# Kernel optimization log

Hardware: AMD Instinct MI355X
Metric: run time of the kernel (lower is better)

The kernel has to match this reference:

```python
import jax, jax.numpy as jnp
import numpy as np

N, E = 20000, 200000
HID, NH, L = 128, 8, 7
DH = HID // NH
SCALE = float(np.sqrt(DH))
NNUM = 5
MLP_IN = HID + HID + 8 + 8 + 8 + NNUM  # 285
EPS = 1e-5


def _ln(x, g, b):
    mu = jnp.mean(x, -1, keepdims=True)
    var = jnp.mean((x - mu) ** 2, -1, keepdims=True)
    return (x - mu) * jax.lax.rsqrt(var + EPS) * g + b


def setup_inputs() -> dict:
    key = jax.random.key(0)
    ks = jax.random.split(key, 24)
    f = lambda k, s: (0.05 * jax.random.normal(k, s)).astype(jnp.float32)
    z = lambda s: jnp.zeros(s, jnp.float32)
    o = lambda s: jnp.ones(s, jnp.float32)
    inp = {
        'node_feats': f(ks[0], (N, 2)),
        'numericals': f(ks[1], (E, NNUM)),
        'W_emb': f(ks[2], (2, HID)), 'b_emb': z((HID,)),
        'WQ': f(ks[3], (L, HID, HID)), 'bQ': z((L, HID)),
        'WK': f(ks[4], (L, HID, HID)), 'bK': z((L, HID)),
        'WV': f(ks[5], (L, HID, HID)), 'bV': z((L, HID)),
        'WO': f(ks[6], (L, HID, HID)), 'bO': z((L, HID)),
        'ln1_g': o((L, HID)), 'ln1_b': z((L, HID)),
        'ln2_g': o((L, HID)), 'ln2_b': z((L, HID)),
        'W1': f(ks[7], (L, HID, HID)), 'b1': z((L, HID)),
        'W2': f(ks[8], (L, HID, HID)), 'b2': z((L, HID)),
        'curr_emb': f(ks[9], (15, 8)), 'pay_emb': f(ks[10], (7, 8)),
        'mlp_Wh': f(ks[11], (3, MLP_IN, MLP_IN)), 'mlp_bh': z((3, MLP_IN)),
        'mlp_Wo': f(ks[12], (MLP_IN, 2)), 'mlp_bo': z((2,)),
        'src': jax.random.randint(ks[13], (E,), 0, N, dtype=jnp.int32),
        'dst': jax.random.randint(ks[14], (E,), 0, N, dtype=jnp.int32),
        'payment_currency': jax.random.randint(ks[15], (E,), 0, 15, dtype=jnp.int32),
        'receiving_currency': jax.random.randint(ks[16], (E,), 0, 15, dtype=jnp.int32),
        'payment_format': jax.random.randint(ks[17], (E,), 0, 7, dtype=jnp.int32),
    }
    return inp


def reference(node_feats, numericals, W_emb, b_emb, WQ, bQ, WK, bK, WV, bV, WO, bO,
              ln1_g, ln1_b, ln2_g, ln2_b, W1, b1, W2, b2, curr_emb, pay_emb,
              mlp_Wh, mlp_bh, mlp_Wo, mlp_bo, src, dst,
              payment_currency, receiving_currency, payment_format):
    h = node_feats @ W_emb + b_emb  # [N, HID]
    for l in range(L):
        # --- graph multi-head attention (segment softmax over in-edges of dst) ---
        x = _ln(h, ln1_g[l], ln1_b[l])
        Q = (x @ WQ[l] + bQ[l]).reshape(N, NH, DH)
        K = (x @ WK[l] + bK[l]).reshape(N, NH, DH)
        V = (x @ WV[l] + bV[l]).reshape(N, NH, DH)
        scores = jnp.einsum('ehd,ehd->eh', Q[dst], K[src]) / SCALE  # [E, NH]
        m = jax.ops.segment_max(scores, dst, num_segments=N)        # [N, NH]
        ex = jnp.exp(scores - m[dst])
        den = jax.ops.segment_sum(ex, dst, num_segments=N)
        w = ex / den[dst]                                           # attn weights per edge
        attn = jax.ops.segment_sum(w[:, :, None] * V[src], dst, num_segments=N)
        h = h + attn.reshape(N, HID) @ WO[l] + bO[l]
        # --- FFN ---
        x = _ln(h, ln2_g[l], ln2_b[l])
        h = h + jax.nn.relu(x @ W1[l] + b1[l]) @ W2[l] + b2[l]
    # --- edge classifier ---
    ef = jnp.concatenate([curr_emb[payment_currency], curr_emb[receiving_currency],
                          pay_emb[payment_format], numericals], axis=1)  # [E, 29]
    y = jnp.concatenate([h[src], h[dst], ef], axis=1)  # [E, 285]
    for i in range(3):
        y = jax.nn.relu(y @ mlp_Wh[i] + mlp_bh[i])
    return y @ mlp_Wo + mlp_bo  # [E, 2]
```

## Files before the change

### kernel.cpp

```cpp
#include <hip/hip_runtime.h>

#define HID 128
#define NH 8
#define DH 16
#define NLAYERS 7
#define MLP_IN 285
#define MP 288
#define LDW 296
#define XS 136

typedef short short8 __attribute__((ext_vector_type(8)));
typedef float f32x4 __attribute__((ext_vector_type(4)));
typedef float f32x16 __attribute__((ext_vector_type(16)));
typedef unsigned short ushort8 __attribute__((ext_vector_type(8)));

__device__ inline unsigned short f2bf(float f) {
    union { float f; unsigned int u; } v; v.f = f;
    unsigned int r = v.u + 0x7FFF + ((v.u >> 16) & 1);
    return (unsigned short)(r >> 16);
}
__device__ inline float bf2f(unsigned short u) {
    union { unsigned int u; float f; } v; v.u = ((unsigned int)u) << 16;
    return v.f;
}

__global__ __launch_bounds__(256) void embed_kernel(
    const float* __restrict__ nf, const float* __restrict__ We,
    const float* __restrict__ be, float* __restrict__ h, int N)
{
    int idx = blockIdx.x * 256 + threadIdx.x;
    if (idx >= N * HID) return;
    int n = idx >> 7, j = idx & 127;
    h[idx] = fmaf(nf[n * 2], We[j], fmaf(nf[n * 2 + 1], We[HID + j], be[j]));
}

__global__ __launch_bounds__(256) void prep_nodew_kernel(
    const float* __restrict__ WQ, const float* __restrict__ WK,
    const float* __restrict__ WV, const float* __restrict__ WO,
    const float* __restrict__ W1, const float* __restrict__ W2,
    unsigned short* __restrict__ wnh, unsigned short* __restrict__ wnl)
{
    int idx = blockIdx.x * 256 + threadIdx.x;
    if (idx >= 42 * 32 * 64) return;
    int lane = idx & 63;
    int r = idx >> 6;
    int kt = r & 7; r >>= 3;
    int ct = r & 3; r >>= 2;
    int m = r;
    int l = m / 6, wi = m - l * 6;
    const float* Wb;
    switch (wi) {
        case 0: Wb = WQ; break; case 1: Wb = WK; break; case 2: Wb = WV; break;
        case 3: Wb = WO; break; case 4: Wb = W1; break; default: Wb = W2; break;
    }
    Wb += (size_t)l * HID * HID;
    int n = ct * 32 + (lane & 31);
    int kb = kt * 16 + (lane >> 5) * 8;
    ushort8 vh, vl;
#pragma unroll
    for (int j = 0; j < 8; ++j) {
        float w = Wb[(size_t)(kb + j) * HID + n];
        unsigned short hi = f2bf(w);
        vh[j] = hi;
        vl[j] = f2bf(w - bf2f(hi));
    }
    *(ushort8*)&wnh[(size_t)idx * 8] = vh;
    *(ushort8*)&wnl[(size_t)idx * 8] = vl;
}

#define LOADB(m, BH, BL) do { \
    size_t fb_ = (((size_t)(matbase + (m)) * 32 + (size_t)wave * 8) * 64 + lane) * 8; \
    const unsigned short* Bh_ = wnh + fb_; \
    const unsigned short* Bl_ = wnl + fb_; \
    _Pragma("unroll") \
    for (int kt = 0; kt < 8; ++kt) { \
        BH[kt] = *(const short8*)&Bh_[kt * 512]; \
        BL[kt] = *(const short8*)&Bl_[kt * 512]; \
    } \
} while (0)

#define COMPACC(BH, BL) \
    f32x16 acc = {}; \
    _Pragma("unroll") \
    for (int kt = 0; kt < 8; ++kt) \
        acc = __builtin_amdgcn_mfma_f32_32x32x16_bf16(ah[kt], BH[kt], acc, 0, 0, 0); \
    _Pragma("unroll") \
    for (int kt = 0; kt < 8; ++kt) \
        acc = __builtin_amdgcn_mfma_f32_32x32x16_bf16(al[kt], BH[kt], acc, 0, 0, 0); \
    _Pragma("unroll") \
    for (int kt = 0; kt < 8; ++kt) \
        acc = __builtin_amdgcn_mfma_f32_32x32x16_bf16(ah[kt], BL[kt], acc, 0, 0, 0);

__global__ __launch_bounds__(256, 2) void ln_qkv_mfma(
    const float* __restrict__ h,
    const float* __restrict__ g, const float* __restrict__ bb,
    const unsigned short* __restrict__ wnh, const unsigned short* __restrict__ wnl,
    int matbase,
    const float* __restrict__ bQ, const float* __restrict__ bK, const float* __restrict__ bV,
    float* __restrict__ qo, float* __restrict__ kvo, int M)
{
    __shared__ unsigned short Xh[32][XS];
    __shared__ unsigned short Xl[32][XS];
    int tid = threadIdx.x;
    int lane = tid & 63, wave = tid >> 6;
    int rowBase = blockIdx.x * 32;

    for (int i = 0; i < 8; ++i) {
        int r = wave * 8 + i;
        int row = rowBase + r;
        float a0 = 0.f, a1 = 0.f;
        if (row < M) {
            a0 = h[(size_t)row * HID + lane];
            a1 = h[(size_t)row * HID + 64 + lane];
        }
        float s = a0 + a1;
#pragma unroll
        for (int off = 32; off > 0; off >>= 1) s += __shfl_down(s, off, 64);
        s = __shfl(s, 0, 64);
        float mu = s * (1.0f / 128.0f);
        float d0 = a0 - mu, d1 = a1 - mu;
        float v = d0 * d0 + d1 * d1;
#pragma unroll
        for (int off = 32; off > 0; off >>= 1) v += __shfl_down(v, off, 64);
        v = __shfl(v, 0, 64);
        float rr = rsqrtf(v * (1.0f / 128.0f) + 1e-5f);
        float x0 = d0 * rr * g[lane] + bb[lane];
        float x1 = d1 * rr * g[64 + lane] + bb[64 + lane];
        unsigned short h0 = f2bf(x0), h1 = f2bf(x1);
        Xh[r][lane] = h0;           Xh[r][64 + lane] = h1;
        Xl[r][lane] = f2bf(x0 - bf2f(h0));
        Xl[r][64 + lane] = f2bf(x1 - bf2f(h1));
    }
    __syncthreads();

    int l31 = lane & 31;
    int half = lane >> 5;

    short8 ah[8], al[8];
#pragma unroll
    for (int kt = 0; kt < 8; ++kt) {
        ah[kt] = *(const short8*)&Xh[l31][kt * 16 + half * 8];
        al[kt] = *(const short8*)&Xl[l31][kt * 16 + half * 8];
    }

    int col = wave * 32 + l31;
    int kvpos = (col >> 1) * 4 + (col & 1);

    short8 bh0[8], bl0[8], bh1[8], bl1[8];
    LOADB(0, bh0, bl0);
    LOADB(1, bh1, bl1);
    {
        COMPACC(bh0, bl0);
        float bv = bQ[col];
#pragma unroll
        for (int r = 0; r < 16; ++r) {
            int rowm = (r & 3) + 8 * (r >> 2) + 4 * half;
            int row = rowBase + rowm;
            if (row < M) qo[(size_t)row * HID + col] = acc[r] + bv;
        }
    }
    LOADB(2, bh0, bl0);
    {
        COMPACC(bh1, bl1);
        float bv = bK[col];
#pragma unroll
        for (int r = 0; r < 16; ++r) {
            int rowm = (r & 3) + 8 * (r >> 2) + 4 * half;
            int row = rowBase + rowm;
            if (row < M) kvo[(size_t)row * 256 + kvpos] = acc[r] + bv;
        }
    }
    {
        COMPACC(bh0, bl0);
        float bv = bV[col];
#pragma unroll
        for (int r = 0; r < 16; ++r) {
            int rowm = (r & 3) + 8 * (r >> 2) + 4 * half;
            int row = rowBase + rowm;
            if (row < M) kvo[(size_t)row * 256 + kvpos + 2] = acc[r] + bv;
        }
    }
}

__global__ __launch_bounds__(256, 2) void post_mfma(
    const float* __restrict__ at, const float* __restrict__ hin,
    const unsigned short* __restrict__ wnh, const unsigned short* __restrict__ wnl,
    int matbase,
    const float* __restrict__ bO,
    const float* __restrict__ g2, const float* __restrict__ b2g,
    const float* __restrict__ b1, const float* __restrict__ b2,
    float* __restrict__ hout, int M)
{
    __shared__ unsigned short Ah[32][XS];
    __shared__ unsigned short Al[32][XS];
    __shared__ unsigned short Th[32][XS];
    __shared__ unsigned short Tl[32][XS];
    __shared__ float Hs[32][132];
    int tid = threadIdx.x;
    int lane = tid & 63, wave = tid >> 6;
    int rowBase = blockIdx.x * 32;
    int l31 = lane & 31;
    int half = lane >> 5;

    for (int i = tid; i < 32 * 32; i += 256) {
        int r = i >> 5, c4 = i & 31;
        int row = rowBase + r;
        float4 va = make_float4(0.f, 0.f, 0.f, 0.f), vh = va;
        if (row < M) {
            va = *(const float4*)&at[(size_t)row * HID + c4 * 4];
            vh = *(const float4*)&hin[(size_t)row * HID + c4 * 4];
        }
        const float* vp = (const float*)&va;
#pragma unroll
        for (int q = 0; q < 4; ++q) {
            unsigned short hi = f2bf(vp[q]);
            Ah[r][c4 * 4 + q] = hi;
            Al[r][c4 * 4 + q] = f2bf(vp[q] - bf2f(hi));
        }
        *(float4*)&Hs[r][c4 * 4] = vh;
    }
    __syncthreads();

    int colW = wave * 32 + l31;

    {
        short8 ah[8], al[8];
#pragma unroll
        for (int kt = 0; kt < 8; ++kt) {
            ah[kt] = *(const short8*)&Ah[l31][kt * 16 + half * 8];
            al[kt] = *(const short8*)&Al[l31][kt * 16 + half * 8];
        }
        short8 bh[8], bl[8];
        LOADB(3, bh, bl);
        COMPACC(bh, bl);
        float bv = bO[colW];
#pragma unroll
        for (int r = 0; r < 16; ++r) {
            int rowm = (r & 3) + 8 * (r >> 2) + 4 * half;
            Hs[rowm][colW] += acc[r] + bv;
        }
    }
    __syncthreads();

    for (int i = 0; i < 8; ++i) {
        int r = wave * 8 + i;
        float a0 = Hs[r][lane];
        float a1 = Hs[r][64 + lane];
        float s = a0 + a1;
#pragma unroll
        for (int off = 32; off > 0; off >>= 1) s += __shfl_down(s, off, 64);
        s = __shfl(s, 0, 64);
        float mu = s * (1.0f / 128.0f);
        float d0 = a0 - mu, d1 = a1 - mu;
        float v = d0 * d0 + d1 * d1;
#pragma unroll
        for (int off = 32; off > 0; off >>= 1) v += __shfl_down(v, off, 64);
        v = __shfl(v, 0, 64);
        float rr = rsqrtf(v * (1.0f / 128.0f) + 1e-5f);
        float x0 = d0 * rr * g2[lane] + b2g[lane];
        float x1 = d1 * rr * g2[64 + lane] + b2g[64 + lane];
        unsigned short h0 = f2bf(x0), h1 = f2bf(x1);
        Ah[r][lane] = h0;           Ah[r][64 + lane] = h1;
        Al[r][lane] = f2bf(x0 - bf2f(h0));
        Al[r][64 + lane] = f2bf(x1 - bf2f(h1));
    }
    __syncthreads();

    {
        short8 ah[8], al[8];
#pragma unroll
        for (int kt = 0; kt < 8; ++kt) {
            ah[kt] = *(const short8*)&Ah[l31][kt * 16 + half * 8];
            al[kt] = *(const short8*)&Al[l31][kt * 16 + half * 8];
        }
        short8 bh[8], bl[8];
        LOADB(4, bh, bl);
        COMPACC(bh, bl);
        float bv = b1[colW];
#pragma unroll
        for (int r = 0; r < 16; ++r) {
            int rowm = (r & 3) + 8 * (r >> 2) + 4 * half;
            float t = fmaxf(acc[r] + bv, 0.f);
            unsigned short hi = f2bf(t);
            Th[rowm][colW] = hi;
            Tl[rowm][colW] = f2bf(t - bf2f(hi));
        }
    }
    __syncthreads();

    {
        short8 ah[8], al[8];
#pragma unroll
        for (int kt = 0; kt < 8; ++kt) {
            ah[kt] = *(const short8*)&Th[l31][kt * 16 + half * 8];
            al[kt] = *(const short8*)&Tl[l31][kt * 16 + half * 8];
        }
        short8 bh[8], bl[8];
        LOADB(5, bh, bl);
        COMPACC(bh, bl);
        float bv = b2[colW];
#pragma unroll
        for (int r = 0; r < 16; ++r) {
            int rowm = (r & 3) + 8 * (r >> 2) + 4 * half;
            int row = rowBase + rowm;
            if (row < M)
                hout[(size_t)row * HID + colW] = Hs[rowm][colW] + acc[r] + bv;
        }
    }
}

__global__ __launch_bounds__(256) void deg_kernel(
    const int* __restrict__ dst, int* __restrict__ deg, int E)
{
    int e = blockIdx.x * 256 + threadIdx.x;
    if (e < E) atomicAdd(&deg[dst[e]], 1);
}

__global__ __launch_bounds__(256) void scan_kernel(
    const int* __restrict__ deg, int* __restrict__ rowptr,
    int* __restrict__ cursor, int N)
{
    __shared__ int sums[256];
    int tid = threadIdx.x;
    int chunk = (N + 255) / 256;
    int lo = tid * chunk;
    int hi = lo + chunk; if (hi > N) hi = N;
    int s = 0;
    for (int i = lo; i < hi && i >= 0; ++i) s += deg[i];
    sums[tid] = s;
    __syncthreads();
    for (int off = 1; off < 256; off <<= 1) {
        int v = (tid >= off) ? sums[tid - off] : 0;
        __syncthreads();
        sums[tid] += v;
        __syncthreads();
    }
    int base = (tid == 0) ? 0 : sums[tid - 1];
    for (int i = lo; i < hi; ++i) {
        rowptr[i] = base; cursor[i] = base; base += deg[i];
    }
    if (tid == 255) rowptr[N] = sums[255];
}

__global__ __launch_bounds__(256) void scatter_kernel(
    const int* __restrict__ src, const int* __restrict__ dst,
    int* __restrict__ cursor, int* __restrict__ ssrc, int E)
{
    int e = blockIdx.x * 256 + threadIdx.x;
    if (e < E) {
        int p = atomicAdd(&cursor[dst[e]], 1);
        ssrc[p] = src[e];
    }
}

__global__ __launch_bounds__(256) void attn_fused_kernel(
    const float* __restrict__ q, const float* __restrict__ kv,
    const int* __restrict__ rowptr, const int* __restrict__ ssrc,
    float* __restrict__ at, int N)
{
    int node = blockIdx.x * 4 + (threadIdx.x >> 6);
    int lane = threadIdx.x & 63;
    if (node >= N) return;
    int beg = rowptr[node], end = rowptr[node + 1];
    float2 q2 = *(const float2*)&q[(size_t)node * HID + lane * 2];
    float ax = 0.f, ay = 0.f, den = 0.f;
    int i = beg;
    for (; i + 2 <= end; i += 2) {
        int s0 = ssrc[i], s1 = ssrc[i + 1];
        float4 kv0 = *(const float4*)&kv[(size_t)s0 * 256 + lane * 4];
        float4 kv1 = *(const float4*)&kv[(size_t)s1 * 256 + lane * 4];
        float p0 = fmaf(q2.x, kv0.x, q2.y * kv0.y);
        float p1 = fmaf(q2.x, kv1.x, q2.y * kv1.y);
        p0 += __shfl_xor(p0, 1, 64); p1 += __shfl_xor(p1, 1, 64);
        p0 += __shfl_xor(p0, 2, 64); p1 += __shfl_xor(p1, 2, 64);
        p0 += __shfl_xor(p0, 4, 64); p1 += __shfl_xor(p1, 4, 64);
        float w0 = __expf(p0 * 0.25f);
        float w1 = __expf(p1 * 0.25f);
        den += w0 + w1;
        ax = fmaf(w1, kv1.z, fmaf(w0, kv0.z, ax));
        ay = fmaf(w1, kv1.w, fmaf(w0, kv0.w, ay));
    }
    if (i < end) {
        int s = ssrc[i];
        float4 kv0 = *(const float4*)&kv[(size_t)s * 256 + lane * 4];
        float p0 = fmaf(q2.x, kv0.x, q2.y * kv0.y);
        p0 += __shfl_xor(p0, 1, 64);
        p0 += __shfl_xor(p0, 2, 64);
        p0 += __shfl_xor(p0, 4, 64);
        float w0 = __expf(p0 * 0.25f);
        den += w0;
        ax = fmaf(w0, kv0.z, ax);
        ay = fmaf(w0, kv0.w, ay);
    }
    float inv = (den > 0.f) ? 1.f / den : 0.f;
    float2 o; o.x = ax * inv; o.y = ay * inv;
    *(float2*)&at[(size_t)node * HID + lane * 2] = o;
}

__global__ __launch_bounds__(256) void prep_wp_kernel(
    const float* __restrict__ Wh, unsigned short* __restrict__ wp)
{
    int idx = blockIdx.x * 256 + threadIdx.x;
    if (idx >= 3 * 9 * 18 * 64) return;
    int lane = idx & 63;
    int r = idx >> 6;
    int kt = r % 18; r /= 18;
    int ct = r % 9;
    int layer = r / 9;
    int n = ct * 32 + (lane & 31);
    int kbase = kt * 16 + (lane >> 5) * 8;
    ushort8 val;
#pragma unroll
    for (int j = 0; j < 8; ++j) {
        int k = kbase + j;
        float v = (n < MLP_IN && k < MLP_IN)
            ? Wh[(size_t)layer * MLP_IN * MLP_IN + (size_t)k * MLP_IN + n] : 0.f;
        val[j] = f2bf(v);
    }
    *(ushort8*)&wp[(size_t)idx * 8] = val;
}

__global__ __launch_bounds__(256) void prep_hb_kernel(
    const float* __restrict__ h, unsigned short* __restrict__ hb, int n)
{
    int idx = blockIdx.x * 256 + threadIdx.x;
    if (idx >= n) return;
    hb[idx] = f2bf(h[idx]);
}

#define ELOADH(h, BUF) do { \
    const unsigned short* Wp_ = Wb + (size_t)((h) >> 1) * 9216 + (size_t)((h) & 1) * 9 * 512; \
    _Pragma("unroll") \
    for (int j = 0; j < 9; ++j) BUF[j] = *(const short8*)&Wp_[j * 512]; \
    __builtin_amdgcn_sched_barrier(0); \
} while (0)

__global__ __launch_bounds__(256, 2) void edge_mlp_mfma(
    const unsigned short* __restrict__ hb, const float* __restrict__ ce,
    const float* __restrict__ pe, const float* __restrict__ num,
    const int* __restrict__ src, const int* __restrict__ dst,
    const int* __restrict__ pc, const int* __restrict__ rc,
    const int* __restrict__ pf,
    const unsigned short* __restrict__ wp, const float* __restrict__ bh,
    const float* __restrict__ Wo, const float* __restrict__ bo,
    float* __restrict__ out, int E)
{
    __shared__ unsigned short y[128 * LDW];
    int tid = threadIdx.x;
    int e0 = blockIdx.x * 128;

    for (int i = tid; i < 128 * 36; i += 256) {
        int t = i / 36;
        int c = i - t * 36;
        int e = e0 + t;
        if (e >= E) e = E - 1;
        ushort8 val;
        if (c < 16) {
            val = *(const ushort8*)&hb[(size_t)src[e] * HID + c * 8];
        } else if (c < 32) {
            val = *(const ushort8*)&hb[(size_t)dst[e] * HID + (c - 16) * 8];
        } else if (c == 32) {
            const float* p = &ce[pc[e] * 8];
#pragma unroll
            for (int j = 0; j < 8; ++j) val[j] = f2bf(p[j]);
        } else if (c == 33) {
            const float* p = &ce[rc[e] * 8];
#pragma unroll
            for (int j = 0; j < 8; ++j) val[j] = f2bf(p[j]);
        } else if (c == 34) {
            const float* p = &pe[pf[e] * 8];
#pragma unroll
            for (int j = 0; j < 8; ++j) val[j] = f2bf(p[j]);
        } else {
            const float* p = &num[(size_t)e * 5];
#pragma unroll
            for (int j = 0; j < 5; ++j) val[j] = f2bf(p[j]);
            val[5] = 0; val[6] = 0; val[7] = 0;
        }
        *(ushort8*)&y[t * LDW + c * 8] = val;
    }
    __syncthreads();

    int wave = tid >> 6;
    int lane = tid & 63;
    int l31 = lane & 31;
    int half = lane >> 5;
    int rowA = wave * 32 + l31;

    for (int layer = 0; layer < 3; ++layer) {
        const unsigned short* __restrict__ Wl = wp + (size_t)layer * 9 * 18 * 64 * 8;
        const float* __restrict__ bias = bh + layer * MLP_IN;
        const unsigned short* Wb = Wl + (size_t)lane * 8;

        short8 afr[18];
#pragma unroll
        for (int kt = 0; kt < 18; ++kt)
            afr[kt] = *(const short8*)&y[rowA * LDW + kt * 16 + half * 8];
        __syncthreads();

        short8 bA[9], bB[9];
        ELOADH(0, bA);
#pragma unroll
        for (int ct = 0; ct < 9; ++ct) {
            f32x16 acc = {};
            ELOADH(2 * ct + 1, bB);
#pragma unroll
            for (int j = 0; j < 9; ++j)
                acc = __builtin_amdgcn_mfma_f32_32x32x16_bf16(afr[j], bA[j], acc, 0, 0, 0);
            if (ct < 8) ELOADH(2 * ct + 2, bA);
#pragma unroll
            for (int j = 0; j < 9; ++j)
                acc = __builtin_amdgcn_mfma_f32_32x32x16_bf16(afr[9 + j], bB[j], acc, 0, 0, 0);
            int col = ct * 32 + l31;
            if (col < MLP_IN) {
                float bv = bias[col];
#pragma unroll
                for (int r = 0; r < 16; ++r) {
                    int rowm = (r & 3) + 8 * (r >> 2) + 4 * half;
                    y[(wave * 32 + rowm) * LDW + col] = f2bf(fmaxf(acc[r] + bv, 0.f));
                }
            }
        }
        __syncthreads();
    }

    {
        int t = tid >> 1, oc = tid & 1;
        int e = e0 + t;
        if (e < E) {
            const unsigned short* yr = &y[t * LDW];
            float p0 = 0.f, p1 = 0.f, p2 = 0.f, p3 = 0.f;
            for (int kc = 0; kc < 35; ++kc) {
                ushort8 yv = *(const ushort8*)&yr[kc * 8];
                int kb = kc * 8;
                p0 = fmaf(bf2f(yv[0]), Wo[(kb + 0) * 2 + oc], p0);
                p1 = fmaf(bf2f(yv[1]), Wo[(kb + 1) * 2 + oc], p1);
                p2 = fmaf(bf2f(yv[2]), Wo[(kb + 2) * 2 + oc], p2);
                p3 = fmaf(bf2f(yv[3]), Wo[(kb + 3) * 2 + oc], p3);
                p0 = fmaf(bf2f(yv[4]), Wo[(kb + 4) * 2 + oc], p0);
                p1 = fmaf(bf2f(yv[5]), Wo[(kb + 5) * 2 + oc], p1);
                p2 = fmaf(bf2f(yv[6]), Wo[(kb + 6) * 2 + oc], p2);
                p3 = fmaf(bf2f(yv[7]), Wo[(kb + 7) * 2 + oc], p3);
            }
            float acc = bo[oc] + (p0 + p1) + (p2 + p3);
            for (int k = 280; k < MLP_IN; ++k)
                acc = fmaf(bf2f(yr[k]), Wo[k * 2 + oc], acc);
            out[(size_t)e * 2 + oc] = acc;
        }
    }
}

extern "C" void kernel_launch(void* const* d_in, const int* in_sizes, int n_in,
                              void* d_out, int out_size, void* d_ws, size_t ws_size,
                              hipStream_t stream)
{
    const float* node_feats = (const float*)d_in[0];
    const float* numericals = (const float*)d_in[1];
    const float* W_emb = (const float*)d_in[2];
    const float* b_emb = (const float*)d_in[3];
    const float* WQ = (const float*)d_in[4];
    const float* bQ = (const float*)d_in[5];
    const float* WK = (const float*)d_in[6];
    const float* bK = (const float*)d_in[7];
    const float* WV = (const float*)d_in[8];
    const float* bV = (const float*)d_in[9];
    const float* WO = (const float*)d_in[10];
    const float* bO = (const float*)d_in[11];
    const float* ln1_g = (const float*)d_in[12];
    const float* ln1_b = (const float*)d_in[13];
    const float* ln2_g = (const float*)d_in[14];
    const float* ln2_b = (const float*)d_in[15];
    const float* W1 = (const float*)d_in[16];
    const float* b1 = (const float*)d_in[17];
    const float* W2 = (const float*)d_in[18];
    const float* b2 = (const float*)d_in[19];
    const float* curr_emb = (const float*)d_in[20];
    const float* pay_emb = (const float*)d_in[21];
    const float* mlp_Wh = (const float*)d_in[22];
    const float* mlp_bh = (const float*)d_in[23];
    const float* mlp_Wo = (const float*)d_in[24];
    const float* mlp_bo = (const float*)d_in[25];
    const int* src = (const int*)d_in[26];
    const int* dst = (const int*)d_in[27];
    const int* pc = (const int*)d_in[28];
    const int* rc = (const int*)d_in[29];
    const int* pf = (const int*)d_in[30];

    const int N = in_sizes[0] / 2;
    const int E = in_sizes[26];

    float* ws = (float*)d_ws;
    float* h   = ws;
    float* qb  = h   + (size_t)N * HID;
    float* kvb = qb  + (size_t)N * HID;
    float* at  = kvb + (size_t)N * HID * 2;
    unsigned short* hb = (unsigned short*)(at + (size_t)N * HID);
    unsigned short* wpk = hb + (size_t)N * HID;
    unsigned short* wnh = wpk + (size_t)3 * 9 * 18 * 64 * 8;
    unsigned short* wnl = wnh + (size_t)42 * 32 * 64 * 8;
    int* rowptr = (int*)(wnl + (size_t)42 * 32 * 64 * 8);
    int* deg    = rowptr + (N + 1);
    int* cursor = deg + N;
    int* ssrc   = cursor + N;

    prep_wp_kernel<<<(3 * 9 * 18 * 64 + 255) / 256, 256, 0, stream>>>(mlp_Wh, wpk);
    prep_nodew_kernel<<<(42 * 32 * 64 + 255) / 256, 256, 0, stream>>>(
        WQ, WK, WV, WO, W1, W2, wnh, wnl);

    embed_kernel<<<(N * HID + 255) / 256, 256, 0, stream>>>(node_feats, W_emb, b_emb, h, N);

    hipMemsetAsync(deg, 0, (size_t)N * sizeof(int), stream);
    deg_kernel<<<(E + 255) / 256, 256, 0, stream>>>(dst, deg, E);
    scan_kernel<<<1, 256, 0, stream>>>(deg, rowptr, cursor, N);
    scatter_kernel<<<(E + 255) / 256, 256, 0, stream>>>(src, dst, cursor, ssrc, E);

    int nodeBlocks = (N + 31) / 32;

    for (int l = 0; l < NLAYERS; ++l) {
        ln_qkv_mfma<<<nodeBlocks, 256, 0, stream>>>(
            h, ln1_g + l * HID, ln1_b + l * HID,
            wnh, wnl, l * 6,
            bQ + l * HID, bK + l * HID, bV + l * HID,
            qb, kvb, N);

        attn_fused_kernel<<<(N + 3) / 4, 256, 0, stream>>>(qb, kvb, rowptr, ssrc, at, N);

        post_mfma<<<nodeBlocks, 256, 0, stream>>>(
            at, h, wnh, wnl, l * 6,
            bO + l * HID,
            ln2_g + l * HID, ln2_b + l * HID,
            b1 + l * HID, b2 + l * HID,
            h, N);
    }

    prep_hb_kernel<<<(N * HID + 255) / 256, 256, 0, stream>>>(h, hb, N * HID);

    edge_mlp_mfma<<<(E + 127) / 128, 256, 0, stream>>>(
        hb, curr_emb, pay_emb, numericals, src, dst, pc, rc, pf,
        wpk, mlp_bh, mlp_Wo, mlp_bo, (float*)d_out, E);
}
```

Baseline: 1.063 ms.

## Fuse attention, output/FFN and next-layer LN+QKV into one per-layer kernel

```diff
diff --git a/kernel.cpp b/kernel.cpp
--- a/kernel.cpp
+++ b/kernel.cpp
@@ -182,14 +182,19 @@
     }
 }
 
-__global__ __launch_bounds__(256, 2) void post_mfma(
-    const float* __restrict__ at, const float* __restrict__ hin,
+__global__ __launch_bounds__(256, 2) void attn_post_qkv(
+    const float* __restrict__ qin, const float* __restrict__ kvin,
+    const int* __restrict__ rowptr, const int* __restrict__ ssrc,
+    float* __restrict__ h,
     const unsigned short* __restrict__ wnh, const unsigned short* __restrict__ wnl,
     int matbase,
     const float* __restrict__ bO,
     const float* __restrict__ g2, const float* __restrict__ b2g,
     const float* __restrict__ b1, const float* __restrict__ b2,
-    float* __restrict__ hout, int M)
+    int doQKV,
+    const float* __restrict__ g1n, const float* __restrict__ b1n,
+    const float* __restrict__ bQn, const float* __restrict__ bKn, const float* __restrict__ bVn,
+    float* __restrict__ qo, float* __restrict__ kvo, int M)
 {
     __shared__ unsigned short Ah[32][XS];
     __shared__ unsigned short Al[32][XS];
@@ -205,19 +210,54 @@
     for (int i = tid; i < 32 * 32; i += 256) {
         int r = i >> 5, c4 = i & 31;
         int row = rowBase + r;
-        float4 va = make_float4(0.f, 0.f, 0.f, 0.f), vh = va;
-        if (row < M) {
-            va = *(const float4*)&at[(size_t)row * HID + c4 * 4];
-            vh = *(const float4*)&hin[(size_t)row * HID + c4 * 4];
-        }
-        const float* vp = (const float*)&va;
-#pragma unroll
-        for (int q = 0; q < 4; ++q) {
-            unsigned short hi = f2bf(vp[q]);
-            Ah[r][c4 * 4 + q] = hi;
-            Al[r][c4 * 4 + q] = f2bf(vp[q] - bf2f(hi));
-        }
+        float4 vh = (row < M) ? *(const float4*)&h[(size_t)row * HID + c4 * 4]
+                              : make_float4(0.f, 0.f, 0.f, 0.f);
         *(float4*)&Hs[r][c4 * 4] = vh;
+    }
+
+    for (int nn = 0; nn < 8; ++nn) {
+        int r = nn * 4 + wave;
+        int node = rowBase + r;
+        float ax = 0.f, ay = 0.f, den = 0.f;
+        if (node < M) {
+            float2 q2 = *(const float2*)&qin[(size_t)node * HID + lane * 2];
+            int beg = rowptr[node], end = rowptr[node + 1];
+            int i = beg;
+            for (; i + 2 <= end; i += 2) {
+                int s0 = ssrc[i], s1 = ssrc[i + 1];
+                float4 kv0 = *(const float4*)&kvin[(size_t)s0 * 256 + lane * 4];
+                float4 kv1 = *(const float4*)&kvin[(size_t)s1 * 256 + lane * 4];
+                float p0 = fmaf(q2.x, kv0.x, q2.y * kv0.y);
+                float p1 = fmaf(q2.x, kv1.x, q2.y * kv1.y);
+                p0 += __shfl_xor(p0, 1, 64); p1 += __shfl_xor(p1, 1, 64);
+                p0 += __shfl_xor(p0, 2, 64); p1 += __shfl_xor(p1, 2, 64);
+                p0 += __shfl_xor(p0, 4, 64); p1 += __shfl_xor(p1, 4, 64);
+                float w0 = __expf(p0 * 0.25f);
+                float w1 = __expf(p1 * 0.25f);
+                den += w0 + w1;
+                ax = fmaf(w1, kv1.z, fmaf(w0, kv0.z, ax));
+                ay = fmaf(w1, kv1.w, fmaf(w0, kv0.w, ay));
+            }
+            if (i < end) {
+                int s = ssrc[i];
+                float4 kv0 = *(const float4*)&kvin[(size_t)s * 256 + lane * 4];
+                float p0 = fmaf(q2.x, kv0.x, q2.y * kv0.y);
+                p0 += __shfl_xor(p0, 1, 64);
+                p0 += __shfl_xor(p0, 2, 64);
+                p0 += __shfl_xor(p0, 4, 64);
+                float w0 = __expf(p0 * 0.25f);
+                den += w0;
+                ax = fmaf(w0, kv0.z, ax);
+                ay = fmaf(w0, kv0.w, ay);
+            }
+        }
+        float inv = (den > 0.f) ? 1.f / den : 0.f;
+        float ox = ax * inv, oy = ay * inv;
+        unsigned short hx = f2bf(ox), hy = f2bf(oy);
+        Ah[r][lane * 2]     = hx;
+        Ah[r][lane * 2 + 1] = hy;
+        Al[r][lane * 2]     = f2bf(ox - bf2f(hx));
+        Al[r][lane * 2 + 1] = f2bf(oy - bf2f(hy));
     }
     __syncthreads();
 
@@ -303,8 +343,81 @@
         for (int r = 0; r < 16; ++r) {
             int rowm = (r & 3) + 8 * (r >> 2) + 4 * half;
             int row = rowBase + rowm;
-            if (row < M)
-                hout[(size_t)row * HID + colW] = Hs[rowm][colW] + acc[r] + bv;
+            float hv = Hs[rowm][colW] + acc[r] + bv;
+            Hs[rowm][colW] = hv;
+            if (row < M) h[(size_t)row * HID + colW] = hv;
+        }
+    }
+
+    if (!doQKV) return;
+    __syncthreads();
+
+    for (int i = 0; i < 8; ++i) {
+        int r = wave * 8 + i;
+        float a0 = Hs[r][lane];
+        float a1 = Hs[r][64 + lane];
+        float s = a0 + a1;
+#pragma unroll
+        for (int off = 32; off > 0; off >>= 1) s += __shfl_down(s, off, 64);
+        s = __shfl(s, 0, 64);
+        float mu = s * (1.0f / 128.0f);
+        float d0 = a0 - mu, d1 = a1 - mu;
+        float v = d0 * d0 + d1 * d1;
+#pragma unroll
+        for (int off = 32; off > 0; off >>= 1) v += __shfl_down(v, off, 64);
+        v = __shfl(v, 0, 64);
+        float rr = rsqrtf(v * (1.0f / 128.0f) + 1e-5f);
+        float x0 = d0 * rr * g1n[lane] + b1n[lane];
+        float x1 = d1 * rr * g1n[64 + lane] + b1n[64 + lane];
+        unsigned short h0 = f2bf(x0), h1 = f2bf(x1);
+        Ah[r][lane] = h0;           Ah[r][64 + lane] = h1;
+        Al[r][lane] = f2bf(x0 - bf2f(h0));
+        Al[r][64 + lane] = f2bf(x1 - bf2f(h1));
+    }
+    __syncthreads();
+
+    {
+        short8 ah[8], al[8];
+#pragma unroll
+        for (int kt = 0; kt < 8; ++kt) {
+            ah[kt] = *(const short8*)&Ah[l31][kt * 16 + half * 8];
+            al[kt] = *(const short8*)&Al[l31][kt * 16 + half * 8];
+        }
+        int col = colW;
+        int kvpos = (col >> 1) * 4 + (col & 1);
+        short8 bh0[8], bl0[8], bh1[8], bl1[8];
+        LOADB(6, bh0, bl0);
+        LOADB(7, bh1, bl1);
+        {
+            COMPACC(bh0, bl0);
+            float bv = bQn[col];
+#pragma unroll
+            for (int r = 0; r < 16; ++r) {
+                int rowm = (r & 3) + 8 * (r >> 2) + 4 * half;
+                int row = rowBase + rowm;
+                if (row < M) qo[(size_t)row * HID + col] = acc[r] + bv;
+            }
+        }
+        LOADB(8, bh0, bl0);
+        {
+            COMPACC(bh1, bl1);
+            float bv = bKn[col];
+#pragma unroll
+            for (int r = 0; r < 16; ++r) {
+                int rowm = (r & 3) + 8 * (r >> 2) + 4 * half;
+                int row = rowBase + rowm;
+                if (row < M) kvo[(size_t)row * 256 + kvpos] = acc[r] + bv;
+            }
+        }
+        {
+            COMPACC(bh0, bl0);
+            float bv = bVn[col];
+#pragma unroll
+            for (int r = 0; r < 16; ++r) {
+                int rowm = (r & 3) + 8 * (r >> 2) + 4 * half;
+                int row = rowBase + rowm;
+                if (row < M) kvo[(size_t)row * 256 + kvpos + 2] = acc[r] + bv;
+            }
         }
     }
 }
@@ -351,50 +464,6 @@
         int p = atomicAdd(&cursor[dst[e]], 1);
         ssrc[p] = src[e];
     }
-}
-
-__global__ __launch_bounds__(256) void attn_fused_kernel(
-    const float* __restrict__ q, const float* __restrict__ kv,
-    const int* __restrict__ rowptr, const int* __restrict__ ssrc,
-    float* __restrict__ at, int N)
-{
-    int node = blockIdx.x * 4 + (threadIdx.x >> 6);
-    int lane = threadIdx.x & 63;
-    if (node >= N) return;
-    int beg = rowptr[node], end = rowptr[node + 1];
-    float2 q2 = *(const float2*)&q[(size_t)node * HID + lane * 2];
-    float ax = 0.f, ay = 0.f, den = 0.f;
-    int i = beg;
-    for (; i + 2 <= end; i += 2) {
-        int s0 = ssrc[i], s1 = ssrc[i + 1];
-        float4 kv0 = *(const float4*)&kv[(size_t)s0 * 256 + lane * 4];
-        float4 kv1 = *(const float4*)&kv[(size_t)s1 * 256 + lane * 4];
-        float p0 = fmaf(q2.x, kv0.x, q2.y * kv0.y);
-        float p1 = fmaf(q2.x, kv1.x, q2.y * kv1.y);
-        p0 += __shfl_xor(p0, 1, 64); p1 += __shfl_xor(p1, 1, 64);
-        p0 += __shfl_xor(p0, 2, 64); p1 += __shfl_xor(p1, 2, 64);
-        p0 += __shfl_xor(p0, 4, 64); p1 += __shfl_xor(p1, 4, 64);
-        float w0 = __expf(p0 * 0.25f);
-        float w1 = __expf(p1 * 0.25f);
-        den += w0 + w1;
-        ax = fmaf(w1, kv1.z, fmaf(w0, kv0.z, ax));
-        ay = fmaf(w1, kv1.w, fmaf(w0, kv0.w, ay));
-    }
-    if (i < end) {
-        int s = ssrc[i];
-        float4 kv0 = *(const float4*)&kv[(size_t)s * 256 + lane * 4];
-        float p0 = fmaf(q2.x, kv0.x, q2.y * kv0.y);
-        p0 += __shfl_xor(p0, 1, 64);
-        p0 += __shfl_xor(p0, 2, 64);
-        p0 += __shfl_xor(p0, 4, 64);
-        float w0 = __expf(p0 * 0.25f);
-        den += w0;
-        ax = fmaf(w0, kv0.z, ax);
-        ay = fmaf(w0, kv0.w, ay);
-    }
-    float inv = (den > 0.f) ? 1.f / den : 0.f;
-    float2 o; o.x = ax * inv; o.y = ay * inv;
-    *(float2*)&at[(size_t)node * HID + lane * 2] = o;
 }
 
 __global__ __launch_bounds__(256) void prep_wp_kernel(
@@ -428,11 +497,26 @@
     hb[idx] = f2bf(h[idx]);
 }
 
-#define ELOADH(h, BUF) do { \
-    const unsigned short* Wp_ = Wb + (size_t)((h) >> 1) * 9216 + (size_t)((h) & 1) * 9 * 512; \
+#define ELOADB(ct, BUF) do { \
+    const unsigned short* Wp_ = Wb + (size_t)(ct) * 9216; \
     _Pragma("unroll") \
-    for (int j = 0; j < 9; ++j) BUF[j] = *(const short8*)&Wp_[j * 512]; \
-    __builtin_amdgcn_sched_barrier(0); \
+    for (int kt = 0; kt < 18; ++kt) BUF[kt] = *(const short8*)&Wp_[kt * 512]; \
+} while (0)
+
+#define EMFMA(ct, BUF) do { \
+    f32x16 acc = {}; \
+    _Pragma("unroll") \
+    for (int kt = 0; kt < 18; ++kt) \
+        acc = __builtin_amdgcn_mfma_f32_32x32x16_bf16(afr[kt], BUF[kt], acc, 0, 0, 0); \
+    int col_ = (ct) * 32 + l31; \
+    if (col_ < MLP_IN) { \
+        float bv_ = bias[col_]; \
+        _Pragma("unroll") \
+        for (int r = 0; r < 16; ++r) { \
+            int rowm_ = (r & 3) + 8 * (r >> 2) + 4 * half; \
+            y[(wave * 32 + rowm_) * LDW + col_] = f2bf(fmaxf(acc[r] + bv_, 0.f)); \
+        } \
+    } \
 } while (0)
 
 __global__ __launch_bounds__(256, 2) void edge_mlp_mfma(
@@ -498,29 +582,16 @@
             afr[kt] = *(const short8*)&y[rowA * LDW + kt * 16 + half * 8];
         __syncthreads();
 
-        short8 bA[9], bB[9];
-        ELOADH(0, bA);
-#pragma unroll
-        for (int ct = 0; ct < 9; ++ct) {
-            f32x16 acc = {};
-            ELOADH(2 * ct + 1, bB);
-#pragma unroll
-            for (int j = 0; j < 9; ++j)
-                acc = __builtin_amdgcn_mfma_f32_32x32x16_bf16(afr[j], bA[j], acc, 0, 0, 0);
-            if (ct < 8) ELOADH(2 * ct + 2, bA);
-#pragma unroll
-            for (int j = 0; j < 9; ++j)
-                acc = __builtin_amdgcn_mfma_f32_32x32x16_bf16(afr[9 + j], bB[j], acc, 0, 0, 0);
-            int col = ct * 32 + l31;
-            if (col < MLP_IN) {
-                float bv = bias[col];
-#pragma unroll
-                for (int r = 0; r < 16; ++r) {
-                    int rowm = (r & 3) + 8 * (r >> 2) + 4 * half;
-                    y[(wave * 32 + rowm) * LDW + col] = f2bf(fmaxf(acc[r] + bv, 0.f));
-                }
-            }
-        }
+        short8 bA[18], bB[18];
+        ELOADB(0, bA);
+#pragma unroll
+        for (int cp = 0; cp < 4; ++cp) {
+            ELOADB(cp * 2 + 1, bB);
+            EMFMA(cp * 2, bA);
+            ELOADB(cp * 2 + 2, bA);
+            EMFMA(cp * 2 + 1, bB);
+        }
+        EMFMA(8, bA);
         __syncthreads();
     }
 
@@ -590,11 +661,11 @@
     const int E = in_sizes[26];
 
     float* ws = (float*)d_ws;
-    float* h   = ws;
-    float* qb  = h   + (size_t)N * HID;
-    float* kvb = qb  + (size_t)N * HID;
-    float* at  = kvb + (size_t)N * HID * 2;
-    unsigned short* hb = (unsigned short*)(at + (size_t)N * HID);
+    float* h    = ws;
+    float* q0   = h    + (size_t)N * HID;
+    float* kv0  = q0   + (size_t)N * HID;
+    float* kv1  = kv0  + (size_t)N * HID * 2;
+    unsigned short* hb = (unsigned short*)(kv1 + (size_t)N * HID * 2);
     unsigned short* wpk = hb + (size_t)N * HID;
     unsigned short* wnh = wpk + (size_t)3 * 9 * 18 * 64 * 8;
     unsigned short* wnl = wnh + (size_t)42 * 32 * 64 * 8;
@@ -616,21 +687,22 @@
 
     int nodeBlocks = (N + 31) / 32;
 
+    ln_qkv_mfma<<<nodeBlocks, 256, 0, stream>>>(
+        h, ln1_g, ln1_b, wnh, wnl, 0, bQ, bK, bV, q0, kv0, N);
+
     for (int l = 0; l < NLAYERS; ++l) {
-        ln_qkv_mfma<<<nodeBlocks, 256, 0, stream>>>(
-            h, ln1_g + l * HID, ln1_b + l * HID,
-            wnh, wnl, l * 6,
-            bQ + l * HID, bK + l * HID, bV + l * HID,
-            qb, kvb, N);
-
-        attn_fused_kernel<<<(N + 3) / 4, 256, 0, stream>>>(qb, kvb, rowptr, ssrc, at, N);
-
-        post_mfma<<<nodeBlocks, 256, 0, stream>>>(
-            at, h, wnh, wnl, l * 6,
+        const float* kvi = (l & 1) ? kv1 : kv0;
+        float* kvo_ = (l & 1) ? kv0 : kv1;
+        int nl = (l < NLAYERS - 1) ? l + 1 : 0;
+        attn_post_qkv<<<nodeBlocks, 256, 0, stream>>>(
+            q0, kvi, rowptr, ssrc, h, wnh, wnl, l * 6,
             bO + l * HID,
             ln2_g + l * HID, ln2_b + l * HID,
             b1 + l * HID, b2 + l * HID,
-            h, N);
+            (l < NLAYERS - 1) ? 1 : 0,
+            ln1_g + nl * HID, ln1_b + nl * HID,
+            bQ + nl * HID, bK + nl * HID, bV + nl * HID,
+            q0, kvo_, N);
     }
 
     prep_hb_kernel<<<(N * HID + 255) / 256, 256, 0, stream>>>(h, hb, N * HID);
```

Result: slower. 1.273 ms (+19.8%).
